# Kernel tuning notes

Measured on AMD Instinct MI355X. Metric: run time of the kernel, lower is better.

## Reference

```python
import jax, jax.numpy as jnp
import numpy as np

N = 100000
IN_C = 128
HID = 8
HEADS = 8
OUT_C = 16
NEG_SLOPE = 0.2  # PyG GATConv default leaky_relu slope
EPS = 1e-16


def setup_inputs() -> dict:
    key = jax.random.key(0)
    ks = jax.random.split(key, 10)
    E = 1600000
    x = jax.random.normal(ks[0], (N, IN_C), dtype=jnp.float32)
    edge_index = jax.random.randint(ks[1], (2, E), 0, N, dtype=jnp.int64)
    g = lambda k, shape: jax.random.normal(k, shape, dtype=jnp.float32) * 0.1
    # layer 1: in -> hid, heads=HEADS, concat
    W1 = g(ks[2], (IN_C, HEADS * HID))
    att_src1 = g(ks[3], (HEADS, HID))
    att_dst1 = g(ks[4], (HEADS, HID))
    b1 = jnp.zeros((HEADS * HID,), jnp.float32)
    # layer 2: hid*heads -> out, heads=1, concat=False (mean)
    W2 = g(ks[5], (HEADS * HID, 1 * OUT_C))
    att_src2 = g(ks[6], (1, OUT_C))
    att_dst2 = g(ks[7], (1, OUT_C))
    b2 = jnp.zeros((OUT_C,), jnp.float32)
    return {"x": x, "edge_index": edge_index, "W1": W1, "att_src1": att_src1,
            "att_dst1": att_dst1, "b1": b1, "W2": W2, "att_src2": att_src2,
            "att_dst2": att_dst2, "b2": b2}


def gat_conv(x, src, dst, W, att_src, att_dst, bias, concat):
    # x: [N, F_in]; src/dst: [E] (self-loops already included)
    H, C = att_src.shape
    h = (x @ W).reshape(N, H, C)                      # [N, H, C]
    a_src = jnp.sum(h * att_src, axis=-1)             # [N, H]
    a_dst = jnp.sum(h * att_dst, axis=-1)             # [N, H]
    alpha = a_src[src] + a_dst[dst]                   # [E, H]
    alpha = jax.nn.leaky_relu(alpha, NEG_SLOPE)
    # segment softmax over incoming edges of each destination node
    amax = jax.ops.segment_max(alpha, dst, num_segments=N)
    alpha = jnp.exp(alpha - amax[dst])
    asum = jax.ops.segment_sum(alpha, dst, num_segments=N)
    alpha = alpha / (asum[dst] + EPS)                 # [E, H]
    # (attention dropout skipped: eval mode)
    out = jax.ops.segment_sum(h[src] * alpha[:, :, None], dst, num_segments=N)  # [N, H, C]
    out = out.reshape(N, H * C) if concat else out.mean(axis=1)
    return out + bias


def reference(x, edge_index, W1, att_src1, att_dst1, b1, W2, att_src2, att_dst2, b2):
    # PyG GATConv adds self-loops by default
    loop = jnp.arange(N, dtype=edge_index.dtype)
    src = jnp.concatenate([edge_index[0], loop])
    dst = jnp.concatenate([edge_index[1], loop])
    h = gat_conv(x, src, dst, W1, att_src1, att_dst1, b1, concat=True)
    h = jax.nn.relu(h)
    out = gat_conv(h, src, dst, W2, att_src2, att_dst2, b2, concat=False)
    return jax.nn.relu(out)
```

## Files before the change

kernel.cpp:

```cpp
#include <hip/hip_runtime.h>
#include <hip/hip_fp16.h>

#define IN_C 128
#define NEG 0.2f
#define GAT_EPS 1e-16f
#define B_N 128
#define NB_MAX 1024
#define TILE 8192
#define GEMM_BLKS 1024

typedef _Float16 half8 __attribute__((ext_vector_type(8)));
typedef float f32x4 __attribute__((ext_vector_type(4)));

static __device__ inline unsigned f2h(float f) {
    _Float16 h = (_Float16)f;
    unsigned short u;
    __builtin_memcpy(&u, &h, 2);
    return (unsigned)u;
}

__global__ __launch_bounds__(256) void k1_kernel(
    const float* __restrict__ x, const float* __restrict__ W1,
    const float* __restrict__ att_s1, const float* __restrict__ att_d1,
    float* __restrict__ hp, __half* __restrict__ a_src1, float* __restrict__ a_dst1,
    const int* __restrict__ ei, int* __restrict__ bucketCnt,
    int E, int Etot, int NB, int N)
{
    __shared__ __align__(16) char smem[34304];
    int tid = threadIdx.x;

    if ((int)blockIdx.x >= GEMM_BLKS) {
        int* hist = (int*)smem;
        for (int i = tid; i < NB; i += 256) hist[i] = 0;
        __syncthreads();
        int base = ((int)blockIdx.x - GEMM_BLKS) * TILE;
        for (int k = tid; k < TILE; k += 256) {
            int e = base + k;
            if (e < Etot) {
                int dst = (e < E) ? ei[E + e] : (e - E);
                atomicAdd(&hist[dst >> 7], 1);
            }
        }
        __syncthreads();
        for (int i = tid; i < NB; i += 256)
            if (hist[i]) atomicAdd(&bucketCnt[i], hist[i]);
        return;
    }

    _Float16* bfrag = (_Float16*)smem;
    float* csbase   = (float*)(smem + 16384);
    float* attS     = (float*)(smem + 16384 + 17408);
    float* attD     = attS + 64;
    if (tid < 64) { attS[tid] = att_s1[tid]; attD[tid] = att_d1[tid]; }
    for (int idx = tid; idx < 8192; idx += 256) {
        int f = idx >> 9;
        int l = (idx >> 3) & 63;
        int j = idx & 7;
        int k0 = f >> 2, nt = f & 3;
        int row = k0 * 32 + ((l >> 4) << 3) + j;
        int col = (nt << 4) + (l & 15);
        bfrag[idx] = (_Float16)W1[row * 64 + col];
    }
    __syncthreads();

    int lane = tid & 63, wid = tid >> 6;
    float* csw = csbase + wid * (16 * 68);
    int mrow = lane & 15;
    int kgrp = lane >> 4;
    const half8* bf8 = (const half8*)bfrag;
    int ntiles = (N + 15) >> 4;
    for (int tile = ((int)blockIdx.x << 2) + wid; tile < ntiles; tile += (GEMM_BLKS << 2)) {
        int n0 = tile << 4;
        f32x4 acc0 = {0,0,0,0}, acc1 = {0,0,0,0}, acc2 = {0,0,0,0}, acc3 = {0,0,0,0};
        int arow = n0 + mrow; if (arow >= N) arow = N - 1;
        const float* xr = x + (size_t)arow * IN_C + (kgrp << 3);
        #pragma unroll
        for (int k0 = 0; k0 < 4; ++k0) {
            float4 xa = *(const float4*)(xr + k0 * 32);
            float4 xb = *(const float4*)(xr + k0 * 32 + 4);
            half8 a;
            a[0] = (_Float16)xa.x; a[1] = (_Float16)xa.y;
            a[2] = (_Float16)xa.z; a[3] = (_Float16)xa.w;
            a[4] = (_Float16)xb.x; a[5] = (_Float16)xb.y;
            a[6] = (_Float16)xb.z; a[7] = (_Float16)xb.w;
            acc0 = __builtin_amdgcn_mfma_f32_16x16x32_f16(a, bf8[(k0 * 4 + 0) * 64 + lane], acc0, 0, 0, 0);
            acc1 = __builtin_amdgcn_mfma_f32_16x16x32_f16(a, bf8[(k0 * 4 + 1) * 64 + lane], acc1, 0, 0, 0);
            acc2 = __builtin_amdgcn_mfma_f32_16x16x32_f16(a, bf8[(k0 * 4 + 2) * 64 + lane], acc2, 0, 0, 0);
            acc3 = __builtin_amdgcn_mfma_f32_16x16x32_f16(a, bf8[(k0 * 4 + 3) * 64 + lane], acc3, 0, 0, 0);
        }
        #pragma unroll
        for (int r = 0; r < 4; ++r) {
            int row = (kgrp << 2) + r;
            csw[row * 68 +  0 + mrow] = acc0[r];
            csw[row * 68 + 16 + mrow] = acc1[r];
            csw[row * 68 + 32 + mrow] = acc2[r];
            csw[row * 68 + 48 + mrow] = acc3[r];
        }
        asm volatile("s_waitcnt lgkmcnt(0)" ::: "memory");
        {
            int node = lane >> 2, cq = lane & 3;
            int n = n0 + node;
            if (n < N) {
                const float* src = &csw[node * 68 + (cq << 4)];
                float4 v0 = *(const float4*)(src);
                float4 v1 = *(const float4*)(src + 4);
                float4 v2 = *(const float4*)(src + 8);
                float4 v3 = *(const float4*)(src + 12);
                unsigned pk[8];
                pk[0] = f2h(v0.x) | (f2h(v0.y) << 16);
                pk[1] = f2h(v0.z) | (f2h(v0.w) << 16);
                pk[2] = f2h(v1.x) | (f2h(v1.y) << 16);
                pk[3] = f2h(v1.z) | (f2h(v1.w) << 16);
                pk[4] = f2h(v2.x) | (f2h(v2.y) << 16);
                pk[5] = f2h(v2.z) | (f2h(v2.w) << 16);
                pk[6] = f2h(v3.x) | (f2h(v3.y) << 16);
                pk[7] = f2h(v3.z) | (f2h(v3.w) << 16);
                char* dst = (char*)(hp + (size_t)n * 32) + (cq << 5);
                ((int4*)dst)[0] = *(int4*)&pk[0];
                ((int4*)dst)[1] = *(int4*)&pk[4];
            }
        }
        #pragma unroll
        for (int pr = 0; pr < 2; ++pr) {
            int node = (pr << 3) + (lane >> 3), head = lane & 7;
            int n = n0 + node;
            if (n < N) {
                float s = 0.f, d = 0.f;
                #pragma unroll
                for (int c = 0; c < 8; ++c) {
                    float v = csw[node * 68 + (head << 3) + c];
                    s = fmaf(v, attS[(head << 3) + c], s);
                    d = fmaf(v, attD[(head << 3) + c], d);
                }
                a_src1[n * 8 + head] = __float2half(s);
                a_dst1[n * 8 + head] = d;
            }
        }
    }
}

__global__ __launch_bounds__(256) void bucket_scan_kernel(
    const int* __restrict__ cnt, int* __restrict__ base, int* __restrict__ cur,
    int* __restrict__ rowstart, int NB, int N, int Etot)
{
    int t = threadIdx.x;
    int v[4]; int s = 0;
    #pragma unroll
    for (int k = 0; k < 4; ++k) { int i = t * 4 + k; v[k] = (i < NB) ? cnt[i] : 0; s += v[k]; }
    int tsum = s;
    int lane = t & 63, wid = t >> 6;
    for (int off = 1; off < 64; off <<= 1) {
        int u = __shfl_up(s, off);
        if (lane >= off) s += u;
    }
    __shared__ int wsH[4];
    if (lane == 63) wsH[wid] = s;
    __syncthreads();
    int woff = 0;
    for (int w = 0; w < wid; ++w) woff += wsH[w];
    int excl = woff + (s - tsum);
    #pragma unroll
    for (int k = 0; k < 4; ++k) {
        int i = t * 4 + k;
        if (i < NB) {
            base[i] = excl; cur[i] = excl;
            if (i == NB - 1) base[NB] = excl + v[k];
            excl += v[k];
        }
    }
    if (t == 0) rowstart[N] = Etot;
}

__global__ __launch_bounds__(256) void partition_kernel(
    const int* __restrict__ ei, int* __restrict__ bucketCur,
    unsigned* __restrict__ ebuf, int E, int Etot, int NB)
{
    __shared__ int lcnt[NB_MAX];
    __shared__ int lbase[NB_MAX];
    int t = threadIdx.x;
    for (int i = t; i < NB; i += 256) lcnt[i] = 0;
    __syncthreads();
    int base = blockIdx.x * TILE;
    for (int k = t; k < TILE; k += 256) {
        int e = base + k;
        if (e < Etot) {
            int dst = (e < E) ? ei[E + e] : (e - E);
            atomicAdd(&lcnt[dst >> 7], 1);
        }
    }
    __syncthreads();
    for (int i = t; i < NB; i += 256) {
        int c = lcnt[i];
        lbase[i] = c ? atomicAdd(&bucketCur[i], c) : 0;
    }
    __syncthreads();
    for (int i = t; i < NB; i += 256) lcnt[i] = 0;
    __syncthreads();
    for (int k = t; k < TILE; k += 256) {
        int e = base + k;
        if (e < Etot) {
            int src, dst;
            if (e < E) { src = ei[e]; dst = ei[E + e]; }
            else       { src = dst = e - E; }
            int b = dst >> 7;
            int r = atomicAdd(&lcnt[b], 1);
            ebuf[lbase[b] + r] = ((unsigned)(dst & (B_N - 1)) << 25) | (unsigned)src;
        }
    }
}

__global__ __launch_bounds__(256) void bucket_sort_kernel(
    const unsigned* __restrict__ ebuf, const int* __restrict__ bucketBase,
    int* __restrict__ rowstart, int* __restrict__ esrc, int N)
{
    __shared__ int lhist[B_N];
    __shared__ int lstart[B_N];
    __shared__ int wsum1;
    int blk = blockIdx.x, t = threadIdx.x;
    int e0 = bucketBase[blk], e1 = bucketBase[blk + 1];
    if (t < B_N) lhist[t] = 0;
    __syncthreads();
    for (int k = e0 + t; k < e1; k += 256)
        atomicAdd(&lhist[ebuf[k] >> 25], 1);
    __syncthreads();
    int lane = t & 63;
    if (t < B_N) {
        int s = lhist[t];
        for (int off = 1; off < 64; off <<= 1) {
            int u = __shfl_up(s, off);
            if (lane >= off) s += u;
        }
        lstart[t] = s;
        if (t == 63) wsum1 = s;
    }
    __syncthreads();
    if (t < B_N) {
        int s = lstart[t];
        if (t >= 64) s += wsum1;
        int excl = s - lhist[t];
        lstart[t] = excl;
        int n = blk * B_N + t;
        if (n < N) rowstart[n] = e0 + excl;
    }
    __syncthreads();
    if (t < B_N) lhist[t] = 0;
    __syncthreads();
    for (int k = e0 + t; k < e1; k += 256) {
        unsigned pk = ebuf[k];
        int d = pk >> 25;
        int r = atomicAdd(&lhist[d], 1);
        esrc[e0 + lstart[d] + r] = (int)(pk & 0x1FFFFFF);
    }
}

__global__ __launch_bounds__(256) void agg1_kernel(
    const int* __restrict__ esrc, const int* __restrict__ rowstart,
    const float* __restrict__ hp, const __half* __restrict__ a_src1,
    const float* __restrict__ a_dst1, const float* __restrict__ b1,
    __half* __restrict__ h2, int N)
{
    int wslot = (blockIdx.x * 256 + threadIdx.x) >> 6;
    int nw = (gridDim.x * 256) >> 6;
    int lane = threadIdx.x & 63;
    int half = lane >> 5, c2 = lane & 31;
    int h = c2 >> 2;
    for (int base = wslot * 2; base < N; base += nw * 2) {
        int n = base + half;
        bool act = (n < N);
        int nn = act ? n : 0;
        int p = rowstart[nn], end = act ? rowstart[nn + 1] : 0;
        float ad = a_dst1[nn * 8 + h];
        float ax = 0.f, ay = 0.f, wsum = 0.f;
        for (; p + 3 < end; p += 4) {
            int s0 = esrc[p], s1 = esrc[p + 1], s2 = esrc[p + 2], s3 = esrc[p + 3];
            float a0 = __half2float(a_src1[s0 * 8 + h]) + ad;
            float a1 = __half2float(a_src1[s1 * 8 + h]) + ad;
            float a2 = __half2float(a_src1[s2 * 8 + h]) + ad;
            float a3 = __half2float(a_src1[s3 * 8 + h]) + ad;
            __half2 q0 = ((const __half2*)(hp + (size_t)s0 * 32))[c2];
            __half2 q1 = ((const __half2*)(hp + (size_t)s1 * 32))[c2];
            __half2 q2 = ((const __half2*)(hp + (size_t)s2 * 32))[c2];
            __half2 q3 = ((const __half2*)(hp + (size_t)s3 * 32))[c2];
            a0 = (a0 > 0.f) ? a0 : NEG * a0;
            a1 = (a1 > 0.f) ? a1 : NEG * a1;
            a2 = (a2 > 0.f) ? a2 : NEG * a2;
            a3 = (a3 > 0.f) ? a3 : NEG * a3;
            float w0 = __expf(a0), w1 = __expf(a1), w2 = __expf(a2), w3 = __expf(a3);
            ax = fmaf(w0, __low2float(q0), ax);  ay = fmaf(w0, __high2float(q0), ay);
            ax = fmaf(w1, __low2float(q1), ax);  ay = fmaf(w1, __high2float(q1), ay);
            ax = fmaf(w2, __low2float(q2), ax);  ay = fmaf(w2, __high2float(q2), ay);
            ax = fmaf(w3, __low2float(q3), ax);  ay = fmaf(w3, __high2float(q3), ay);
            wsum += (w0 + w1) + (w2 + w3);
        }
        for (; p < end; ++p) {
            int s0 = esrc[p];
            float a0 = __half2float(a_src1[s0 * 8 + h]) + ad;
            __half2 q0 = ((const __half2*)(hp + (size_t)s0 * 32))[c2];
            a0 = (a0 > 0.f) ? a0 : NEG * a0;
            float w0 = __expf(a0);
            ax = fmaf(w0, __low2float(q0), ax);
            ay = fmaf(w0, __high2float(q0), ay);
            wsum += w0;
        }
        if (act) {
            float inv = 1.f / (wsum + GAT_EPS);
            float2 bb = *(const float2*)(b1 + 2 * c2);
            float vx = fmaf(ax, inv, bb.x);
            float vy = fmaf(ay, inv, bb.y);
            vx = vx > 0.f ? vx : 0.f;
            vy = vy > 0.f ? vy : 0.f;
            ((__half2*)(h2 + (size_t)n * 64))[c2] =
                __halves2half2(__float2half(vx), __float2half(vy));
        }
    }
}

__global__ __launch_bounds__(256) void gemm2_kernel(
    const __half* __restrict__ h2, const float* __restrict__ W2,
    const float* __restrict__ att_s2, const float* __restrict__ att_d2,
    __half* __restrict__ h2w, float* __restrict__ a_src2, float* __restrict__ a_dst2, int N)
{
    __shared__ _Float16 bfrag[2 * 512];
    __shared__ float cs[4][16 * 20];
    int tid = threadIdx.x;
    for (int idx = tid; idx < 1024; idx += 256) {
        int f = idx >> 9, l = (idx >> 3) & 63, j = idx & 7;
        int row = f * 32 + ((l >> 4) << 3) + j;
        int col = l & 15;
        bfrag[idx] = (_Float16)W2[row * 16 + col];
    }
    __syncthreads();
    int lane = tid & 63, wid = tid >> 6;
    int mrow = lane & 15, kgrp = lane >> 4;
    float* csw = &cs[wid][0];
    const half8* bf8 = (const half8*)bfrag;
    int ech = (lane & 3) << 2;
    float as0 = att_s2[ech], as1 = att_s2[ech + 1], as2 = att_s2[ech + 2], as3 = att_s2[ech + 3];
    float ad0 = att_d2[ech], ad1 = att_d2[ech + 1], ad2 = att_d2[ech + 2], ad3 = att_d2[ech + 3];
    int ntiles = (N + 15) >> 4;
    for (int tile = (blockIdx.x << 2) + wid; tile < ntiles; tile += (gridDim.x << 2)) {
        int n0 = tile << 4;
        f32x4 acc = {0, 0, 0, 0};
        int arow = n0 + mrow; if (arow >= N) arow = N - 1;
        const half8* h2r = (const half8*)(h2 + (size_t)arow * 64 + (kgrp << 3));
        acc = __builtin_amdgcn_mfma_f32_16x16x32_f16(h2r[0], bf8[lane], acc, 0, 0, 0);
        acc = __builtin_amdgcn_mfma_f32_16x16x32_f16(h2r[4], bf8[64 + lane], acc, 0, 0, 0);
        #pragma unroll
        for (int r = 0; r < 4; ++r)
            csw[((kgrp << 2) + r) * 20 + mrow] = acc[r];
        asm volatile("s_waitcnt lgkmcnt(0)" ::: "memory");
        int node = lane >> 2;
        int n = n0 + node;
        if (n < N) {
            float4 v = *(const float4*)&csw[node * 20 + ech];
            unsigned pk0 = f2h(v.x) | (f2h(v.y) << 16);
            unsigned pk1 = f2h(v.z) | (f2h(v.w) << 16);
            *(int2*)((char*)(h2w + (size_t)n * 16) + (ech << 1)) = make_int2((int)pk0, (int)pk1);
            float s = fmaf(v.x, as0, fmaf(v.y, as1, fmaf(v.z, as2, v.w * as3)));
            float d = fmaf(v.x, ad0, fmaf(v.y, ad1, fmaf(v.z, ad2, v.w * ad3)));
            s += __shfl_xor(s, 1); d += __shfl_xor(d, 1);
            s += __shfl_xor(s, 2); d += __shfl_xor(d, 2);
            if ((lane & 3) == 0) { a_src2[n] = s; a_dst2[n] = d; }
        }
    }
}

__global__ __launch_bounds__(256) void agg2_kernel(
    const int* __restrict__ esrc, const int* __restrict__ rowstart,
    const __half* __restrict__ h2w, const float* __restrict__ a_src2,
    const float* __restrict__ a_dst2, const float* __restrict__ b2,
    float* __restrict__ out, int N)
{
    int wslot = (blockIdx.x * 256 + threadIdx.x) >> 6;
    int nw = (gridDim.x * 256) >> 6;
    int lane = threadIdx.x & 63;
    int oct = lane >> 3, c2 = lane & 7;
    for (int base = wslot * 8; base < N; base += nw * 8) {
        int n = base + oct;
        bool act = (n < N);
        int nn = act ? n : 0;
        int p = rowstart[nn], end = act ? rowstart[nn + 1] : 0;
        float ad = a_dst2[nn];
        float ax = 0.f, ay = 0.f, wsum = 0.f;
        for (; p + 3 < end; p += 4) {
            int s0 = esrc[p], s1 = esrc[p + 1], s2 = esrc[p + 2], s3 = esrc[p + 3];
            float a0 = a_src2[s0] + ad;
            float a1 = a_src2[s1] + ad;
            float a2 = a_src2[s2] + ad;
            float a3 = a_src2[s3] + ad;
            __half2 q0 = ((const __half2*)(h2w + (size_t)s0 * 16))[c2];
            __half2 q1 = ((const __half2*)(h2w + (size_t)s1 * 16))[c2];
            __half2 q2 = ((const __half2*)(h2w + (size_t)s2 * 16))[c2];
            __half2 q3 = ((const __half2*)(h2w + (size_t)s3 * 16))[c2];
            a0 = (a0 > 0.f) ? a0 : NEG * a0;
            a1 = (a1 > 0.f) ? a1 : NEG * a1;
            a2 = (a2 > 0.f) ? a2 : NEG * a2;
            a3 = (a3 > 0.f) ? a3 : NEG * a3;
            float w0 = __expf(a0), w1 = __expf(a1), w2 = __expf(a2), w3 = __expf(a3);
            ax = fmaf(w0, __low2float(q0), ax);  ay = fmaf(w0, __high2float(q0), ay);
            ax = fmaf(w1, __low2float(q1), ax);  ay = fmaf(w1, __high2float(q1), ay);
            ax = fmaf(w2, __low2float(q2), ax);  ay = fmaf(w2, __high2float(q2), ay);
            ax = fmaf(w3, __low2float(q3), ax);  ay = fmaf(w3, __high2float(q3), ay);
            wsum += (w0 + w1) + (w2 + w3);
        }
        for (; p < end; ++p) {
            int s0 = esrc[p];
            float a0 = a_src2[s0] + ad;
            __half2 q0 = ((const __half2*)(h2w + (size_t)s0 * 16))[c2];
            a0 = (a0 > 0.f) ? a0 : NEG * a0;
            float w0 = __expf(a0);
            ax = fmaf(w0, __low2float(q0), ax);
            ay = fmaf(w0, __high2float(q0), ay);
            wsum += w0;
        }
        if (act) {
            float inv = 1.f / (wsum + GAT_EPS);
            float2 bb = *(const float2*)(b2 + 2 * c2);
            float2 o;
            o.x = fmaf(ax, inv, bb.x);
            o.y = fmaf(ay, inv, bb.y);
            o.x = o.x > 0.f ? o.x : 0.f;
            o.y = o.y > 0.f ? o.y : 0.f;
            ((float2*)(out + (size_t)n * 16))[c2] = o;
        }
    }
}

extern "C" void kernel_launch(void* const* d_in, const int* in_sizes, int n_in,
                              void* d_out, int out_size, void* d_ws, size_t ws_size,
                              hipStream_t stream)
{
    const float* x      = (const float*)d_in[0];
    const int*   ei     = (const int*)  d_in[1];
    const float* W1     = (const float*)d_in[2];
    const float* att_s1 = (const float*)d_in[3];
    const float* att_d1 = (const float*)d_in[4];
    const float* b1     = (const float*)d_in[5];
    const float* W2     = (const float*)d_in[6];
    const float* att_s2 = (const float*)d_in[7];
    const float* att_d2 = (const float*)d_in[8];
    const float* b2     = (const float*)d_in[9];
    float* out = (float*)d_out;

    int N = in_sizes[0] / IN_C;
    int E = in_sizes[1] / 2;
    int Etot = E + N;
    int NB = (N + B_N - 1) / B_N;

    float* ws = (float*)d_ws;
    float*  hp      = ws;
    __half* a_src1  = (__half*)(hp + (size_t)N * 32);
    float*  a_dst1  = (float*)a_src1 + (size_t)N * 4;
    __half* h2      = (__half*)(a_dst1 + (size_t)N * 8);
    __half* h2w     = (__half*)((float*)h2 + (size_t)N * 32);
    float*  a_src2  = (float*)h2w + (size_t)N * 8;
    float*  a_dst2  = a_src2 + (size_t)N;
    int* rowstart   = (int*)(a_dst2 + (size_t)N);
    int* bucketCnt  = rowstart   + (N + 1);
    int* bucketBase = bucketCnt  + NB_MAX;
    int* bucketCur  = bucketBase + NB_MAX + 1;
    int* esrc       = bucketCur  + NB_MAX;
    unsigned* ebuf  = (unsigned*)(esrc + Etot);

    int egrid = (Etot + TILE - 1) / TILE;

    hipMemsetAsync(bucketCnt, 0, NB_MAX * sizeof(int), stream);
    k1_kernel<<<GEMM_BLKS + egrid, 256, 0, stream>>>(
        x, W1, att_s1, att_d1, hp, a_src1, a_dst1, ei, bucketCnt, E, Etot, NB, N);
    bucket_scan_kernel<<<1, 256, 0, stream>>>(bucketCnt, bucketBase, bucketCur,
                                              rowstart, NB, N, Etot);
    partition_kernel<<<egrid, 256, 0, stream>>>(ei, bucketCur, ebuf, E, Etot, NB);
    bucket_sort_kernel<<<NB, 256, 0, stream>>>(ebuf, bucketBase, rowstart, esrc, N);

    agg1_kernel<<<2048, 256, 0, stream>>>(esrc, rowstart, hp, a_src1, a_dst1, b1, h2, N);

    gemm2_kernel<<<1024, 256, 0, stream>>>(h2, W2, att_s2, att_d2, h2w, a_src2, a_dst2, N);
    agg2_kernel<<<1024, 256, 0, stream>>>(esrc, rowstart, h2w, a_src2, a_dst2, b2, out, N);
}
```

Before: 176.4 us.

## Fuse layer-1 aggregation with layer-2 GEMM and co-schedule partition with GEMM1

Moves the bucket-count pass into its own kernel and co-schedules the edge partition pass with the layer-1 MFMA GEMM in one launch, instead of co-scheduling the count pass with it. Fuses agg1 and gemm2 so that the aggregated hidden features stay in shared memory and go straight into the W2 MFMA, removing the h2 global round trip and one launch. Inside the unrolled aggregation loop, each lane computes one of the 32 edge-head attention weights and the weights are shared by shuffles, instead of every lane recomputing all four exps. The GEMM block count also drops. The risks are lower occupancy in the fused kernel from its extra shared memory and fixed per-group work, and the change in which pass overlaps the GEMM.

```diff
diff --git a/kernel.cpp b/kernel.cpp
--- a/kernel.cpp
+++ b/kernel.cpp
@@ -7,7 +7,7 @@
 #define B_N 128
 #define NB_MAX 1024
 #define TILE 8192
-#define GEMM_BLKS 1024
+#define GEMM_BLKS 768
 
 typedef _Float16 half8 __attribute__((ext_vector_type(8)));
 typedef float f32x4 __attribute__((ext_vector_type(4)));
@@ -19,31 +19,100 @@
     return (unsigned)u;
 }
 
-__global__ __launch_bounds__(256) void k1_kernel(
+__global__ __launch_bounds__(256) void bucket_count_kernel(
+    const int* __restrict__ ei, int* __restrict__ bucketCnt, int E, int Etot, int NB)
+{
+    __shared__ int hist[NB_MAX];
+    int t = threadIdx.x;
+    for (int i = t; i < NB; i += 256) hist[i] = 0;
+    __syncthreads();
+    int base = blockIdx.x * TILE;
+    for (int k = t; k < TILE; k += 256) {
+        int e = base + k;
+        if (e < Etot) {
+            int dst = (e < E) ? ei[E + e] : (e - E);
+            atomicAdd(&hist[dst >> 7], 1);
+        }
+    }
+    __syncthreads();
+    for (int i = t; i < NB; i += 256)
+        if (hist[i]) atomicAdd(&bucketCnt[i], hist[i]);
+}
+
+__global__ __launch_bounds__(256) void bucket_scan_kernel(
+    const int* __restrict__ cnt, int* __restrict__ base, int* __restrict__ cur,
+    int* __restrict__ rowstart, int NB, int N, int Etot)
+{
+    int t = threadIdx.x;
+    int v[4]; int s = 0;
+    #pragma unroll
+    for (int k = 0; k < 4; ++k) { int i = t * 4 + k; v[k] = (i < NB) ? cnt[i] : 0; s += v[k]; }
+    int tsum = s;
+    int lane = t & 63, wid = t >> 6;
+    for (int off = 1; off < 64; off <<= 1) {
+        int u = __shfl_up(s, off);
+        if (lane >= off) s += u;
+    }
+    __shared__ int wsH[4];
+    if (lane == 63) wsH[wid] = s;
+    __syncthreads();
+    int woff = 0;
+    for (int w = 0; w < wid; ++w) woff += wsH[w];
+    int excl = woff + (s - tsum);
+    #pragma unroll
+    for (int k = 0; k < 4; ++k) {
+        int i = t * 4 + k;
+        if (i < NB) {
+            base[i] = excl; cur[i] = excl;
+            if (i == NB - 1) base[NB] = excl + v[k];
+            excl += v[k];
+        }
+    }
+    if (t == 0) rowstart[N] = Etot;
+}
+
+__global__ __launch_bounds__(256) void k2_kernel(
     const float* __restrict__ x, const float* __restrict__ W1,
     const float* __restrict__ att_s1, const float* __restrict__ att_d1,
     float* __restrict__ hp, __half* __restrict__ a_src1, float* __restrict__ a_dst1,
-    const int* __restrict__ ei, int* __restrict__ bucketCnt,
-    int E, int Etot, int NB, int N)
+    const int* __restrict__ ei, int* __restrict__ bucketCur, unsigned* __restrict__ ebuf,
+    int E, int Etot, int NB, int N, int egrid)
 {
     __shared__ __align__(16) char smem[34304];
     int tid = threadIdx.x;
 
-    if ((int)blockIdx.x >= GEMM_BLKS) {
-        int* hist = (int*)smem;
-        for (int i = tid; i < NB; i += 256) hist[i] = 0;
+    if ((int)blockIdx.x < egrid) {
+        int* lcnt  = (int*)smem;
+        int* lbase = lcnt + NB_MAX;
+        for (int i = tid; i < NB; i += 256) lcnt[i] = 0;
         __syncthreads();
-        int base = ((int)blockIdx.x - GEMM_BLKS) * TILE;
+        int base = (int)blockIdx.x * TILE;
         for (int k = tid; k < TILE; k += 256) {
             int e = base + k;
             if (e < Etot) {
                 int dst = (e < E) ? ei[E + e] : (e - E);
-                atomicAdd(&hist[dst >> 7], 1);
+                atomicAdd(&lcnt[dst >> 7], 1);
             }
         }
         __syncthreads();
-        for (int i = tid; i < NB; i += 256)
-            if (hist[i]) atomicAdd(&bucketCnt[i], hist[i]);
+        for (int i = tid; i < NB; i += 256) {
+            int c = lcnt[i];
+            lbase[i] = c ? atomicAdd(&bucketCur[i], c) : 0;
+        }
+        __syncthreads();
+        for (int i = tid; i < NB; i += 256) lcnt[i] = 0;
+        __syncthreads();
+        for (int k = tid; k < TILE; k += 256) {
+            int e = base + k;
+            if (e < Etot) {
+                int src, dst;
+                if (e < E) { src = ei[e]; dst = ei[E + e]; }
+                else       { src = dst = e - E; }
+                int b = dst >> 7;
+                int r = atomicAdd(&lcnt[b], 1);
+                ebuf[lbase[b] + r] = ((unsigned)(dst & (B_N - 1)) << 25) | (unsigned)src;
+            }
+        }
         return;
     }
 
@@ -69,7 +138,8 @@
     int kgrp = lane >> 4;
     const half8* bf8 = (const half8*)bfrag;
     int ntiles = (N + 15) >> 4;
-    for (int tile = ((int)blockIdx.x << 2) + wid; tile < ntiles; tile += (GEMM_BLKS << 2)) {
+    int gb = (int)blockIdx.x - egrid;
+    for (int tile = (gb << 2) + wid; tile < ntiles; tile += (GEMM_BLKS << 2)) {
         int n0 = tile << 4;
         f32x4 acc0 = {0,0,0,0}, acc1 = {0,0,0,0}, acc2 = {0,0,0,0}, acc3 = {0,0,0,0};
         int arow = n0 + mrow; if (arow >= N) arow = N - 1;
@@ -139,76 +209,6 @@
     }
 }
 
-__global__ __launch_bounds__(256) void bucket_scan_kernel(
-    const int* __restrict__ cnt, int* __restrict__ base, int* __restrict__ cur,
-    int* __restrict__ rowstart, int NB, int N, int Etot)
-{
-    int t = threadIdx.x;
-    int v[4]; int s = 0;
-    #pragma unroll
-    for (int k = 0; k < 4; ++k) { int i = t * 4 + k; v[k] = (i < NB) ? cnt[i] : 0; s += v[k]; }
-    int tsum = s;
-    int lane = t & 63, wid = t >> 6;
-    for (int off = 1; off < 64; off <<= 1) {
-        int u = __shfl_up(s, off);
-        if (lane >= off) s += u;
-    }
-    __shared__ int wsH[4];
-    if (lane == 63) wsH[wid] = s;
-    __syncthreads();
-    int woff = 0;
-    for (int w = 0; w < wid; ++w) woff += wsH[w];
-    int excl = woff + (s - tsum);
-    #pragma unroll
-    for (int k = 0; k < 4; ++k) {
-        int i = t * 4 + k;
-        if (i < NB) {
-            base[i] = excl; cur[i] = excl;
-            if (i == NB - 1) base[NB] = excl + v[k];
-            excl += v[k];
-        }
-    }
-    if (t == 0) rowstart[N] = Etot;
-}
-
-__global__ __launch_bounds__(256) void partition_kernel(
-    const int* __restrict__ ei, int* __restrict__ bucketCur,
-    unsigned* __restrict__ ebuf, int E, int Etot, int NB)
-{
-    __shared__ int lcnt[NB_MAX];
-    __shared__ int lbase[NB_MAX];
-    int t = threadIdx.x;
-    for (int i = t; i < NB; i += 256) lcnt[i] = 0;
-    __syncthreads();
-    int base = blockIdx.x * TILE;
-    for (int k = t; k < TILE; k += 256) {
-        int e = base + k;
-        if (e < Etot) {
-            int dst = (e < E) ? ei[E + e] : (e - E);
-            atomicAdd(&lcnt[dst >> 7], 1);
-        }
-    }
-    __syncthreads();
-    for (int i = t; i < NB; i += 256) {
-        int c = lcnt[i];
-        lbase[i] = c ? atomicAdd(&bucketCur[i], c) : 0;
-    }
-    __syncthreads();
-    for (int i = t; i < NB; i += 256) lcnt[i] = 0;
-    __syncthreads();
-    for (int k = t; k < TILE; k += 256) {
-        int e = base + k;
-        if (e < Etot) {
-            int src, dst;
-            if (e < E) { src = ei[e]; dst = ei[E + e]; }
-            else       { src = dst = e - E; }
-            int b = dst >> 7;
-            int r = atomicAdd(&lcnt[b], 1);
-            ebuf[lbase[b] + r] = ((unsigned)(dst & (B_N - 1)) << 25) | (unsigned)src;
-        }
-    }
-}
-
 __global__ __launch_bounds__(256) void bucket_sort_kernel(
     const unsigned* __restrict__ ebuf, const int* __restrict__ bucketBase,
     int* __restrict__ rowstart, int* __restrict__ esrc, int N)
@@ -253,104 +253,100 @@
     }
 }
 
-__global__ __launch_bounds__(256) void agg1_kernel(
+__global__ __launch_bounds__(256) void agg1g2_kernel(
     const int* __restrict__ esrc, const int* __restrict__ rowstart,
     const float* __restrict__ hp, const __half* __restrict__ a_src1,
     const float* __restrict__ a_dst1, const float* __restrict__ b1,
-    __half* __restrict__ h2, int N)
-{
-    int wslot = (blockIdx.x * 256 + threadIdx.x) >> 6;
-    int nw = (gridDim.x * 256) >> 6;
-    int lane = threadIdx.x & 63;
-    int half = lane >> 5, c2 = lane & 31;
-    int h = c2 >> 2;
-    for (int base = wslot * 2; base < N; base += nw * 2) {
-        int n = base + half;
-        bool act = (n < N);
-        int nn = act ? n : 0;
-        int p = rowstart[nn], end = act ? rowstart[nn + 1] : 0;
-        float ad = a_dst1[nn * 8 + h];
-        float ax = 0.f, ay = 0.f, wsum = 0.f;
-        for (; p + 3 < end; p += 4) {
-            int s0 = esrc[p], s1 = esrc[p + 1], s2 = esrc[p + 2], s3 = esrc[p + 3];
-            float a0 = __half2float(a_src1[s0 * 8 + h]) + ad;
-            float a1 = __half2float(a_src1[s1 * 8 + h]) + ad;
-            float a2 = __half2float(a_src1[s2 * 8 + h]) + ad;
-            float a3 = __half2float(a_src1[s3 * 8 + h]) + ad;
-            __half2 q0 = ((const __half2*)(hp + (size_t)s0 * 32))[c2];
-            __half2 q1 = ((const __half2*)(hp + (size_t)s1 * 32))[c2];
-            __half2 q2 = ((const __half2*)(hp + (size_t)s2 * 32))[c2];
-            __half2 q3 = ((const __half2*)(hp + (size_t)s3 * 32))[c2];
-            a0 = (a0 > 0.f) ? a0 : NEG * a0;
-            a1 = (a1 > 0.f) ? a1 : NEG * a1;
-            a2 = (a2 > 0.f) ? a2 : NEG * a2;
-            a3 = (a3 > 0.f) ? a3 : NEG * a3;
-            float w0 = __expf(a0), w1 = __expf(a1), w2 = __expf(a2), w3 = __expf(a3);
-            ax = fmaf(w0, __low2float(q0), ax);  ay = fmaf(w0, __high2float(q0), ay);
-            ax = fmaf(w1, __low2float(q1), ax);  ay = fmaf(w1, __high2float(q1), ay);
-            ax = fmaf(w2, __low2float(q2), ax);  ay = fmaf(w2, __high2float(q2), ay);
-            ax = fmaf(w3, __low2float(q3), ax);  ay = fmaf(w3, __high2float(q3), ay);
-            wsum += (w0 + w1) + (w2 + w3);
-        }
-        for (; p < end; ++p) {
-            int s0 = esrc[p];
-            float a0 = __half2float(a_src1[s0 * 8 + h]) + ad;
-            __half2 q0 = ((const __half2*)(hp + (size_t)s0 * 32))[c2];
-            a0 = (a0 > 0.f) ? a0 : NEG * a0;
-            float w0 = __expf(a0);
-            ax = fmaf(w0, __low2float(q0), ax);
-            ay = fmaf(w0, __high2float(q0), ay);
-            wsum += w0;
-        }
-        if (act) {
-            float inv = 1.f / (wsum + GAT_EPS);
-            float2 bb = *(const float2*)(b1 + 2 * c2);
-            float vx = fmaf(ax, inv, bb.x);
-            float vy = fmaf(ay, inv, bb.y);
-            vx = vx > 0.f ? vx : 0.f;
-            vy = vy > 0.f ? vy : 0.f;
-            ((__half2*)(h2 + (size_t)n * 64))[c2] =
-                __halves2half2(__float2half(vx), __float2half(vy));
-        }
-    }
-}
-
-__global__ __launch_bounds__(256) void gemm2_kernel(
-    const __half* __restrict__ h2, const float* __restrict__ W2,
-    const float* __restrict__ att_s2, const float* __restrict__ att_d2,
-    __half* __restrict__ h2w, float* __restrict__ a_src2, float* __restrict__ a_dst2, int N)
-{
-    __shared__ _Float16 bfrag[2 * 512];
+    const float* __restrict__ W2, const float* __restrict__ att_s2,
+    const float* __restrict__ att_d2, __half* __restrict__ h2w,
+    float* __restrict__ a_src2, float* __restrict__ a_dst2, int N)
+{
+    __shared__ _Float16 w2frag[1024];
+    __shared__ _Float16 h2s[4][16][64];
     __shared__ float cs[4][16 * 20];
     int tid = threadIdx.x;
     for (int idx = tid; idx < 1024; idx += 256) {
         int f = idx >> 9, l = (idx >> 3) & 63, j = idx & 7;
         int row = f * 32 + ((l >> 4) << 3) + j;
         int col = l & 15;
-        bfrag[idx] = (_Float16)W2[row * 16 + col];
-    }
-    __syncthreads();
+        w2frag[idx] = (_Float16)W2[row * 16 + col];
+    }
+    __syncthreads();
+
     int lane = tid & 63, wid = tid >> 6;
+    int half = lane >> 5, c2 = lane & 31;
+    int h = c2 >> 2;
+    int ch = c2 & 7;
+    int sbase = half * 32 + h;
+    float2 bb = *(const float2*)(b1 + 2 * c2);
     int mrow = lane & 15, kgrp = lane >> 4;
+    const half8* w2bf8 = (const half8*)w2frag;
     float* csw = &cs[wid][0];
-    const half8* bf8 = (const half8*)bfrag;
     int ech = (lane & 3) << 2;
     float as0 = att_s2[ech], as1 = att_s2[ech + 1], as2 = att_s2[ech + 2], as3 = att_s2[ech + 3];
     float ad0 = att_d2[ech], ad1 = att_d2[ech + 1], ad2 = att_d2[ech + 2], ad3 = att_d2[ech + 3];
-    int ntiles = (N + 15) >> 4;
-    for (int tile = (blockIdx.x << 2) + wid; tile < ntiles; tile += (gridDim.x << 2)) {
-        int n0 = tile << 4;
+
+    int ngroups = (N + 63) >> 6;
+    for (int grp = blockIdx.x; grp < ngroups; grp += gridDim.x) {
+        int wbase = (grp << 6) + (wid << 4);
+        for (int sub = 0; sub < 8; ++sub) {
+            int nloc = (sub << 1) + half;
+            int n = wbase + nloc;
+            bool act = (n < N);
+            int nn = act ? n : 0;
+            int p = rowstart[nn], end = act ? rowstart[nn + 1] : 0;
+            float ad_f = a_dst1[nn * 8 + h];
+            float ad_c = a_dst1[nn * 8 + ch];
+            float ax = 0.f, ay = 0.f, wsum = 0.f;
+            for (; p + 3 < end; p += 4) {
+                int s0 = esrc[p], s1 = esrc[p + 1], s2 = esrc[p + 2], s3 = esrc[p + 3];
+                int se = (c2 & 16) ? ((c2 & 8) ? s3 : s2) : ((c2 & 8) ? s1 : s0);
+                float ac = __half2float(a_src1[se * 8 + ch]) + ad_c;
+                ac = (ac > 0.f) ? ac : NEG * ac;
+                float wl = __expf(ac);
+                float w0 = __shfl(wl, sbase);
+                float w1 = __shfl(wl, sbase + 8);
+                float w2 = __shfl(wl, sbase + 16);
+                float w3 = __shfl(wl, sbase + 24);
+                __half2 q0 = ((const __half2*)(hp + (size_t)s0 * 32))[c2];
+                __half2 q1 = ((const __half2*)(hp + (size_t)s1 * 32))[c2];
+                __half2 q2 = ((const __half2*)(hp + (size_t)s2 * 32))[c2];
+                __half2 q3 = ((const __half2*)(hp + (size_t)s3 * 32))[c2];
+                ax = fmaf(w0, __low2float(q0), ax);  ay = fmaf(w0, __high2float(q0), ay);
+                ax = fmaf(w1, __low2float(q1), ax);  ay = fmaf(w1, __high2float(q1), ay);
+                ax = fmaf(w2, __low2float(q2), ax);  ay = fmaf(w2, __high2float(q2), ay);
+                ax = fmaf(w3, __low2float(q3), ax);  ay = fmaf(w3, __high2float(q3), ay);
+                wsum += (w0 + w1) + (w2 + w3);
+            }
+            for (; p < end; ++p) {
+                int s0 = esrc[p];
+                float a0 = __half2float(a_src1[s0 * 8 + h]) + ad_f;
+                __half2 q0 = ((const __half2*)(hp + (size_t)s0 * 32))[c2];
+                a0 = (a0 > 0.f) ? a0 : NEG * a0;
+                float w0 = __expf(a0);
+                ax = fmaf(w0, __low2float(q0), ax);
+                ay = fmaf(w0, __high2float(q0), ay);
+                wsum += w0;
+            }
+            float inv = 1.f / (wsum + GAT_EPS);
+            float vx = fmaf(ax, inv, bb.x);
+            float vy = fmaf(ay, inv, bb.y);
+            vx = (act && vx > 0.f) ? vx : 0.f;
+            vy = (act && vy > 0.f) ? vy : 0.f;
+            ((__half2*)&h2s[wid][nloc][0])[c2] =
+                __halves2half2(__float2half(vx), __float2half(vy));
+        }
+        asm volatile("s_waitcnt lgkmcnt(0)" ::: "memory");
         f32x4 acc = {0, 0, 0, 0};
-        int arow = n0 + mrow; if (arow >= N) arow = N - 1;
-        const half8* h2r = (const half8*)(h2 + (size_t)arow * 64 + (kgrp << 3));
-        acc = __builtin_amdgcn_mfma_f32_16x16x32_f16(h2r[0], bf8[lane], acc, 0, 0, 0);
-        acc = __builtin_amdgcn_mfma_f32_16x16x32_f16(h2r[4], bf8[64 + lane], acc, 0, 0, 0);
+        const half8* ar = (const half8*)&h2s[wid][mrow][0];
+        acc = __builtin_amdgcn_mfma_f32_16x16x32_f16(ar[kgrp], w2bf8[lane], acc, 0, 0, 0);
+        acc = __builtin_amdgcn_mfma_f32_16x16x32_f16(ar[4 + kgrp], w2bf8[64 + lane], acc, 0, 0, 0);
         #pragma unroll
         for (int r = 0; r < 4; ++r)
             csw[((kgrp << 2) + r) * 20 + mrow] = acc[r];
         asm volatile("s_waitcnt lgkmcnt(0)" ::: "memory");
         int node = lane >> 2;
-        int n = n0 + node;
+        int n = wbase + node;
         if (n < N) {
             float4 v = *(const float4*)&csw[node * 20 + ech];
             unsigned pk0 = f2h(v.x) | (f2h(v.y) << 16);
@@ -451,8 +447,7 @@
     float*  hp      = ws;
     __half* a_src1  = (__half*)(hp + (size_t)N * 32);
     float*  a_dst1  = (float*)a_src1 + (size_t)N * 4;
-    __half* h2      = (__half*)(a_dst1 + (size_t)N * 8);
-    __half* h2w     = (__half*)((float*)h2 + (size_t)N * 32);
+    __half* h2w     = (__half*)(a_dst1 + (size_t)N * 8);
     float*  a_src2  = (float*)h2w + (size_t)N * 8;
     float*  a_dst2  = a_src2 + (size_t)N;
     int* rowstart   = (int*)(a_dst2 + (size_t)N);
@@ -465,15 +460,19 @@
     int egrid = (Etot + TILE - 1) / TILE;
 
     hipMemsetAsync(bucketCnt, 0, NB_MAX * sizeof(int), stream);
-    k1_kernel<<<GEMM_BLKS + egrid, 256, 0, stream>>>(
-        x, W1, att_s1, att_d1, hp, a_src1, a_dst1, ei, bucketCnt, E, Etot, NB, N);
+    bucket_count_kernel<<<egrid, 256, 0, stream>>>(ei, bucketCnt, E, Etot, NB);
     bucket_scan_kernel<<<1, 256, 0, stream>>>(bucketCnt, bucketBase, bucketCur,
                                               rowstart, NB, N, Etot);
-    partition_kernel<<<egrid, 256, 0, stream>>>(ei, bucketCur, ebuf, E, Etot, NB);
+    k2_kernel<<<egrid + GEMM_BLKS, 256, 0, stream>>>(
+        x, W1, att_s1, att_d1, hp, a_src1, a_dst1, ei, bucketCur, ebuf,
+        E, Etot, NB, N, egrid);
     bucket_sort_kernel<<<NB, 256, 0, stream>>>(ebuf, bucketBase, rowstart, esrc, N);
 
-    agg1_kernel<<<2048, 256, 0, stream>>>(esrc, rowstart, hp, a_src1, a_dst1, b1, h2, N);
-
-    gemm2_kernel<<<1024, 256, 0, stream>>>(h2, W2, att_s2, att_d2, h2w, a_src2, a_dst2, N);
+    {
+        int ngroups = (N + 63) >> 6;
+        agg1g2_kernel<<<ngroups, 256, 0, stream>>>(
+            esrc, rowstart, hp, a_src1, a_dst1, b1,
+            W2, att_s2, att_d2, h2w, a_src2, a_dst2, N);
+    }
     agg2_kernel<<<1024, 256, 0, stream>>>(esrc, rowstart, h2w, a_src2, a_dst2, b2, out, N);
 }
```

Measured after the change: 170.6 us. 3.3% less time.
